# Kernel tuning notes

Measured on AMD Instinct MI355X. Metric: run time of the kernel, lower is better.

The kernel has to match this reference:

```python
import jax, jax.numpy as jnp
import numpy as np

N = 100_000   # num_nodes
D = 64        # emb_dim
E = 1_600_000 # num edges (before self loops)
L = 3         # n_layers
NEG_SLOPE = 0.2


def setup_inputs() -> dict:
    key = jax.random.key(0)
    ks = jax.random.split(key, 6)
    edge_index = jax.random.randint(ks[0], (2, E), 0, N, dtype=jnp.int32)
    # xavier-ish init for embedding and per-layer GATConv params
    emb = jax.random.normal(ks[1], (N, D), jnp.float32) * (1.0 / np.sqrt(D))
    W = jax.random.normal(ks[2], (L, D, D), jnp.float32) * (1.0 / np.sqrt(D))
    att_src = jax.random.normal(ks[3], (L, D), jnp.float32) * 0.1
    att_dst = jax.random.normal(ks[4], (L, D), jnp.float32) * 0.1
    bias = jnp.zeros((L, D), jnp.float32)
    return {"edge_index": edge_index, "emb": emb, "W": W,
            "att_src": att_src, "att_dst": att_dst, "bias": bias}


def _gat_layer(x, src, dst, W, a_s, a_d, b):
    # PyG GATConv, heads=1, concat=False, self-loops already in (src, dst)
    h = x @ W                                   # [N, D]
    e_s = h @ a_s                               # [N] per-node src score
    e_d = h @ a_d                               # [N] per-node dst score
    e = jax.nn.leaky_relu(e_s[src] + e_d[dst], NEG_SLOPE)   # [E']
    # segment softmax grouped by destination node (max is detached in PyG)
    m = jax.lax.stop_gradient(jax.ops.segment_max(e, dst, num_segments=N))
    ex = jnp.exp(e - m[dst])
    denom = jax.ops.segment_sum(ex, dst, num_segments=N)
    alpha = ex / (denom[dst] + 1e-16)           # [E']
    out = jax.ops.segment_sum(alpha[:, None] * h[src], dst, num_segments=N)
    return out + b


def reference(edge_index, emb, W, att_src, att_dst, bias):
    loops = jnp.arange(N, dtype=edge_index.dtype)
    src = jnp.concatenate([edge_index[0], loops])
    dst = jnp.concatenate([edge_index[1], loops])
    x = emb
    outs = [x]
    for l in range(L):
        x = jax.nn.elu(_gat_layer(x, src, dst, W[l], att_src[l], att_dst[l], bias[l]))
        outs.append(x)
    return jnp.mean(jnp.stack(outs, axis=0), axis=0)  # [N, D]
```

## Files before the change

kernel.cpp:

```cpp
#include <hip/hip_runtime.h>
#include <hip/hip_bf16.h>


#define BSHIFT 9
#define NPB 512
#define COL_CAP 10240

typedef _Float16 v8h __attribute__((ext_vector_type(8)));
typedef float v4f __attribute__((ext_vector_type(4)));
typedef unsigned short u16x8 __attribute__((ext_vector_type(8)));

__device__ inline float bf2f(unsigned short u) {
    return __uint_as_float(((unsigned int)u) << 16);
}
__device__ inline unsigned short f2bf(float v) {
    __hip_bfloat16 b = __float2bfloat16(v);
    return *reinterpret_cast<unsigned short*>(&b);
}
__device__ inline unsigned short f2h_u(float v) {
    return __builtin_bit_cast(unsigned short, (_Float16)v);
}
__device__ inline float h2f_u(unsigned short u) {
    return (float)__builtin_bit_cast(_Float16, u);
}

__global__ __launch_bounds__(256) void detect_bf16_k(const unsigned int* raw, int* flag, int* ghist) {
    __shared__ int sc;
    if (threadIdx.x == 0) sc = 0;
    ghist[threadIdx.x] = 0;
    __syncthreads();
    int c = 0;
    for (int i = threadIdx.x; i < 4096; i += 256) {
        unsigned int b = (raw[i] >> 8) & 0x7Fu;
        if (b >= 0x3Bu && b <= 0x3Fu) c++;
    }
    atomicAdd(&sc, c);
    __syncthreads();
    if (threadIdx.x == 0) *flag = (sc > 2048) ? 1 : 0;
}

__device__ inline float load_in(const void* p, int i, int isbf) {
    if (isbf) return bf2f(((const unsigned short*)p)[i]);
    return ((const float*)p)[i];
}

__global__ __launch_bounds__(256) void conv_emb_k(const void* emb, unsigned short* x, float* outacc,
                                                  int n, const int* flag) {
    int i = blockIdx.x * 256 + threadIdx.x;
    if (i >= n) return;
    float v = load_in(emb, i, *flag);
    x[i] = f2h_u(v);
    outacc[i] = v;
}

__global__ __launch_bounds__(256) void conv_params_k(const void* W, const void* as_, const void* ad_,
                                                     const void* b_, unsigned short* Wh, float* asf,
                                                     float* adf, float* bf, int nw, int na,
                                                     const int* flag) {
    int i = blockIdx.x * 256 + threadIdx.x;
    int isbf = *flag;
    if (i < nw) Wh[i] = f2h_u(load_in(W, i, isbf));
    if (i < na) {
        asf[i] = load_in(as_, i, isbf);
        adf[i] = load_in(ad_, i, isbf);
        bf[i]  = load_in(b_,  i, isbf);
    }
}


__global__ __launch_bounds__(256) void hist_k(const int* dst, int* ghist, int E) {
    __shared__ int h[256];
    h[threadIdx.x] = 0;
    __syncthreads();
    int cs = blockIdx.x * 4096;
    int ce = min(cs + 4096, E);
    for (int i = cs + threadIdx.x; i < ce; i += 256)
        atomicAdd(&h[dst[i] >> BSHIFT], 1);
    __syncthreads();
    if (h[threadIdx.x]) atomicAdd(&ghist[threadIdx.x], h[threadIdx.x]);
}

__global__ __launch_bounds__(256) void scan_nb_k(const int* ghist, int* pairs_base, int* col_base,
                                                 int* cursor, int* rowptr, int N, int E, int NB) {
    __shared__ int s1[256], s2[256];
    int t = threadIdx.x;
    int hv = (t < NB) ? ghist[t] : 0;
    int npb = (t < NB) ? min(N - (t << BSHIFT), NPB) : 0;
    s1[t] = hv; s2[t] = hv + npb;
    __syncthreads();
    for (int off = 1; off < 256; off <<= 1) {
        int t1 = (t >= off) ? s1[t - off] : 0;
        int t2 = (t >= off) ? s2[t - off] : 0;
        __syncthreads();
        s1[t] += t1; s2[t] += t2;
        __syncthreads();
    }
    if (t < NB) {
        pairs_base[t] = s1[t] - hv;
        cursor[t]     = s1[t] - hv;
        col_base[t]   = s2[t] - (hv + npb);
    }
    if (t == 0) rowptr[N] = E + N;
}

__global__ __launch_bounds__(256) void partition_k(const int* __restrict__ src,
                                                   const int* __restrict__ dst,
                                                   int* cursor, uint2* __restrict__ pairs,
                                                   int E, int NB) {
    __shared__ int cnt[256], base[256], rk[256];
    int t = threadIdx.x;
    cnt[t] = 0; rk[t] = 0;
    __syncthreads();
    int cs = blockIdx.x * 4096;
    int ce = min(cs + 4096, E);
    for (int i = cs + t; i < ce; i += 256)
        atomicAdd(&cnt[dst[i] >> BSHIFT], 1);
    __syncthreads();
    if (t < NB && cnt[t]) base[t] = atomicAdd(&cursor[t], cnt[t]);
    __syncthreads();
    for (int i = cs + t; i < ce; i += 256) {
        int d = dst[i];
        int b = d >> BSHIFT;
        int r = atomicAdd(&rk[b], 1);
        pairs[base[b] + r] = make_uint2((unsigned)src[i], (unsigned)d);
    }
}

__global__ __launch_bounds__(512) void build_k(const uint2* __restrict__ pairs,
                                               const int* __restrict__ ghist,
                                               const int* __restrict__ pairs_base,
                                               const int* __restrict__ col_base,
                                               int* __restrict__ rowptr, int* __restrict__ col,
                                               int N) {
    __shared__ int cnt[512], cnt2[512], sc[512], off[513];
    __shared__ int col_lds[COL_CAP];
    int b = blockIdx.x, t = threadIdx.x;
    int nloc = min(N - (b << BSHIFT), NPB);
    int ne = ghist[b], pb = pairs_base[b], cb = col_base[b];
    cnt[t] = 0; cnt2[t] = 0;
    __syncthreads();
    for (int i = t; i < ne; i += 512)
        atomicAdd(&cnt[pairs[pb + i].y & (NPB - 1)], 1);
    __syncthreads();
    int v = cnt[t] + (t < nloc ? 1 : 0);
    sc[t] = v;
    __syncthreads();
    for (int o = 1; o < 512; o <<= 1) {
        int tv = (t >= o) ? sc[t - o] : 0;
        __syncthreads();
        sc[t] += tv;
        __syncthreads();
    }
    off[t + 1] = sc[t];
    if (t == 0) off[0] = 0;
    __syncthreads();
    if (t < nloc) rowptr[(b << BSHIFT) + t] = cb + off[t];
    int total = off[nloc];
    bool fit = (total <= COL_CAP);
    for (int i = t; i < ne; i += 512) {
        uint2 p = pairs[pb + i];
        int loc = p.y & (NPB - 1);
        int pos = off[loc] + atomicAdd(&cnt2[loc], 1);
        if (fit) col_lds[pos] = (int)p.x;
        else     col[cb + pos] = (int)p.x;
    }
    if (t < nloc) {
        int pos = off[t + 1] - 1;
        int sv = (b << BSHIFT) + t;
        if (fit) col_lds[pos] = sv;
        else     col[cb + pos] = sv;
    }
    __syncthreads();
    if (fit)
        for (int i = t; i < total; i += 512) col[cb + i] = col_lds[i];
}


__global__ __launch_bounds__(256) void gemm_k(const unsigned short* __restrict__ x,
                                              const unsigned short* __restrict__ Wh,
                                              const float* __restrict__ asv,
                                              const float* __restrict__ adv,
                                              unsigned short* __restrict__ h,
                                              float* __restrict__ es, float* __restrict__ ed,
                                              int n, int nblk, int nwaves) {
    int lane = threadIdx.x & 63;
    int gwave = (blockIdx.x * 256 + threadIdx.x) >> 6;
    int c = lane & 15, quad = lane >> 4;

    v8h b[4][2];
    #pragma unroll
    for (int t = 0; t < 4; ++t)
        #pragma unroll
        for (int kf = 0; kf < 2; ++kf)
            #pragma unroll
            for (int j = 0; j < 8; ++j)
                b[t][kf][j] = __builtin_bit_cast(_Float16,
                    Wh[(kf * 32 + quad * 8 + j) * 64 + t * 16 + c]);

    float as4[4], ad4[4];
    #pragma unroll
    for (int t = 0; t < 4; ++t) { as4[t] = asv[t * 16 + c]; ad4[t] = adv[t * 16 + c]; }

    for (int nb = gwave; nb < nblk; nb += nwaves) {
        int base = nb * 16;
        int m = base + c; if (m >= n) m = n - 1;
        const v8h a0 = *(const v8h*)(x + (size_t)m * 64 + quad * 8);
        const v8h a1 = *(const v8h*)(x + (size_t)m * 64 + 32 + quad * 8);
        v4f z = {0.f, 0.f, 0.f, 0.f};
        v4f acc[4];
        #pragma unroll
        for (int t = 0; t < 4; ++t) {
            acc[t] = __builtin_amdgcn_mfma_f32_16x16x32_f16(a0, b[t][0], z, 0, 0, 0);
            acc[t] = __builtin_amdgcn_mfma_f32_16x16x32_f16(a1, b[t][1], acc[t], 0, 0, 0);
        }
        float ps[4], pd[4];
        #pragma unroll
        for (int r = 0; r < 4; ++r) {
            ps[r] = acc[0][r] * as4[0] + acc[1][r] * as4[1] + acc[2][r] * as4[2] + acc[3][r] * as4[3];
            pd[r] = acc[0][r] * ad4[0] + acc[1][r] * ad4[1] + acc[2][r] * ad4[2] + acc[3][r] * ad4[3];
        }
        #pragma unroll
        for (int off = 1; off < 16; off <<= 1)
            #pragma unroll
            for (int r = 0; r < 4; ++r) {
                ps[r] += __shfl_xor(ps[r], off);
                pd[r] += __shfl_xor(pd[r], off);
            }
        #pragma unroll
        for (int t = 0; t < 4; ++t)
            #pragma unroll
            for (int r = 0; r < 4; ++r) {
                int row = base + quad * 4 + r;
                if (row < n) h[(size_t)row * 64 + t * 16 + c] = f2h_u(acc[t][r]);
            }
        if (c == 0) {
            #pragma unroll
            for (int r = 0; r < 4; ++r) {
                int row = base + quad * 4 + r;
                if (row < n) { es[row] = ps[r]; ed[row] = pd[r]; }
            }
        }
    }
}

__device__ inline float elu_f(float v) { return v > 0.f ? v : (__expf(v) - 1.f); }

__global__ __launch_bounds__(256) void agg_k(const unsigned short* __restrict__ h,
                                             const float* __restrict__ es,
                                             const float* __restrict__ ed, const int* __restrict__ rowptr,
                                             const int* __restrict__ col, const float* __restrict__ bias,
                                             unsigned short* __restrict__ x, float* __restrict__ outacc,
                                             void* __restrict__ out, const int* __restrict__ flag,
                                             int write_out, int n) {
    int gw = (blockIdx.x * 256 + threadIdx.x) >> 6;
    int lane = threadIdx.x & 63;
    if (gw >= n) return;
    int start = rowptr[gw], end = rowptr[gw + 1];
    int deg = end - start;
    float edd = ed[gw];

    if (deg <= 64) {
        int c = 0;
        float e = -1e30f;
        if (lane < deg) {
            c = col[start + lane];
            float t = es[c] + edd;
            e = t > 0.f ? t : 0.2f * t;
        }
        float m = e;
        #pragma unroll
        for (int off = 32; off; off >>= 1) m = fmaxf(m, __shfl_xor(m, off));
        float ex = (lane < deg) ? __expf(e - m) : 0.f;
        float sum = ex;
        #pragma unroll
        for (int off = 32; off; off >>= 1) sum += __shfl_xor(sum, off);
        float a = ex / (sum + 1e-16f);

        int g = lane >> 3, j = lane & 7;
        float acc[8];
        #pragma unroll
        for (int i = 0; i < 8; ++i) acc[i] = 0.f;
        for (int t = 0; t < deg; t += 8) {
            int idx = t + g;
            int   s  = __shfl(c, idx);
            float al = __shfl(a, idx);
            if (idx < deg) {
                const u16x8 hv = *(const u16x8*)(h + (size_t)s * 64 + j * 8);
                #pragma unroll
                for (int i = 0; i < 8; ++i)
                    acc[i] = fmaf(al, h2f_u(hv[i]), acc[i]);
            }
        }
        #pragma unroll
        for (int off = 8; off < 64; off <<= 1)
            #pragma unroll
            for (int i = 0; i < 8; ++i)
                acc[i] += __shfl_xor(acc[i], off);

        if (g == 0) {
            size_t base = (size_t)gw * 64 + j * 8;
            float y[8], oa[8];
            #pragma unroll
            for (int i = 0; i < 8; ++i) {
                y[i] = elu_f(acc[i] + bias[j * 8 + i]);
                oa[i] = outacc[base + i] + y[i];
            }
            if (write_out) {
                if (*flag) {
                    u16x8 o;
                    #pragma unroll
                    for (int i = 0; i < 8; ++i) o[i] = f2bf(oa[i] * 0.25f);
                    *(u16x8*)((unsigned short*)out + base) = o;
                } else {
                    float4 o0 = make_float4(oa[0] * 0.25f, oa[1] * 0.25f, oa[2] * 0.25f, oa[3] * 0.25f);
                    float4 o1 = make_float4(oa[4] * 0.25f, oa[5] * 0.25f, oa[6] * 0.25f, oa[7] * 0.25f);
                    *(float4*)((float*)out + base) = o0;
                    *(float4*)((float*)out + base + 4) = o1;
                }
            } else {
                u16x8 xo;
                #pragma unroll
                for (int i = 0; i < 8; ++i) xo[i] = f2h_u(y[i]);
                *(u16x8*)(x + base) = xo;
                float4 o0 = make_float4(oa[0], oa[1], oa[2], oa[3]);
                float4 o1 = make_float4(oa[4], oa[5], oa[6], oa[7]);
                *(float4*)(outacc + base) = o0;
                *(float4*)(outacc + base + 4) = o1;
            }
        }
    } else {
        float m = -1e30f;
        for (int k = start + lane; k < end; k += 64) {
            float e = es[col[k]] + edd;
            e = e > 0.f ? e : 0.2f * e;
            m = fmaxf(m, e);
        }
        #pragma unroll
        for (int off = 32; off; off >>= 1) m = fmaxf(m, __shfl_xor(m, off));
        float sum = 0.f;
        for (int k = start + lane; k < end; k += 64) {
            float e = es[col[k]] + edd;
            e = e > 0.f ? e : 0.2f * e;
            sum += __expf(e - m);
        }
        #pragma unroll
        for (int off = 32; off; off >>= 1) sum += __shfl_xor(sum, off);
        float inv = 1.f / (sum + 1e-16f);
        float acc = 0.f;
        for (int k = start; k < end; ++k) {
            int s = col[k];
            float e = es[s] + edd;
            e = e > 0.f ? e : 0.2f * e;
            float al = __expf(e - m) * inv;
            acc = fmaf(al, h2f_u(h[(size_t)s * 64 + lane]), acc);
        }
        size_t base = (size_t)gw * 64 + lane;
        float y = elu_f(acc + bias[lane]);
        float oa = outacc[base] + y;
        if (write_out) {
            if (*flag) ((unsigned short*)out)[base] = f2bf(oa * 0.25f);
            else       ((float*)out)[base] = oa * 0.25f;
        } else {
            x[base] = f2h_u(y);
            outacc[base] = oa;
        }
    }
}


extern "C" void kernel_launch(void* const* d_in, const int* in_sizes, int n_in,
                              void* d_out, int out_size, void* d_ws, size_t ws_size,
                              hipStream_t stream) {
    const int*  edge = (const int*)d_in[0];
    const void* emb  = d_in[1];
    const void* W    = d_in[2];
    const void* as_  = d_in[3];
    const void* ad_  = d_in[4];
    const void* b_   = d_in[5];

    const int E = in_sizes[0] / 2;
    const int N = in_sizes[1] / 64;
    const int L = in_sizes[2] / 4096;
    const int NB = (N + NPB - 1) >> BSHIFT;
    const size_t N64 = (size_t)N * 64;

    char* p = (char*)d_ws;
    auto take = [&](size_t bytes) { char* r = p; p += (bytes + 255) & ~(size_t)255; return r; };
    unsigned short* x = (unsigned short*)take(N64 * 2);
    unsigned short* h = (unsigned short*)take(N64 * 2);
    float* outacc  = (float*)take(N64 * 4);
    float* es      = (float*)take((size_t)N * 4);
    float* ed      = (float*)take((size_t)N * 4);
    unsigned short* Wh = (unsigned short*)take((size_t)L * 4096 * 2);
    float* asf     = (float*)take((size_t)L * 64 * 4);
    float* adf     = (float*)take((size_t)L * 64 * 4);
    float* bf      = (float*)take((size_t)L * 64 * 4);
    uint2* pairs   = (uint2*)take((size_t)E * 8);
    int* rowptr    = (int*)take((size_t)(N + 1) * 4);
    int* col       = (int*)take((size_t)(E + N) * 4);
    int* ghist     = (int*)take(256 * 4);
    int* pairs_base= (int*)take(256 * 4);
    int* col_base  = (int*)take(256 * 4);
    int* cursor    = (int*)take(256 * 4);
    int* flag      = (int*)take(4);

    const int* srcp = edge;
    const int* dstp = edge + E;
    int nchunk = (E + 4095) / 4096;

    detect_bf16_k<<<1, 256, 0, stream>>>((const unsigned int*)emb, flag, ghist);
    conv_emb_k<<<(int)((N64 + 255) / 256), 256, 0, stream>>>(emb, x, outacc, (int)N64, flag);
    conv_params_k<<<(L * 4096 + 255) / 256, 256, 0, stream>>>(W, as_, ad_, b_, Wh, asf, adf, bf,
                                                              L * 4096, L * 64, flag);

    hist_k<<<nchunk, 256, 0, stream>>>(dstp, ghist, E);
    scan_nb_k<<<1, 256, 0, stream>>>(ghist, pairs_base, col_base, cursor, rowptr, N, E, NB);
    partition_k<<<nchunk, 256, 0, stream>>>(srcp, dstp, cursor, pairs, E, NB);
    build_k<<<NB, 512, 0, stream>>>(pairs, ghist, pairs_base, col_base, rowptr, col, N);

    const int nblk = (N + 15) / 16;
    const int ggrid = 400;
    for (int l = 0; l < L; ++l) {
        gemm_k<<<ggrid, 256, 0, stream>>>(x, Wh + (size_t)l * 4096, asf + l * 64, adf + l * 64,
                                          h, es, ed, N, nblk, ggrid * 4);
        agg_k<<<(N + 3) / 4, 256, 0, stream>>>(h, es, ed, rowptr, col, bf + l * 64, x, outacc,
                                               d_out, flag, (l == L - 1) ? 1 : 0, N);
    }
}
```

Baseline: 371.6 us.

## Fold attention vectors into GEMM, store per-layer fp16 outputs, finalize mean once

Precomputes W·att_src and W·att_dst on the device and packs them as an extra MFMA B-fragment, so the GEMM yields es/ed directly instead of needing per-row shuffle reductions. Weights are pre-laid-out in fragment order so each lane loads them with vector loads. The fp32 running-mean accumulator read-modify-write in every aggregation is replaced by per-layer fp16 outputs, which one finalize kernel averages; x2 reuses the pairs buffer. It also unrolls the edge gather by two and raises the GEMM grid. The trade-off is that the mean is now computed from fp16-rounded values, and there is one extra kernel launch.

```diff
diff --git a/kernel.cpp b/kernel.cpp
--- a/kernel.cpp
+++ b/kernel.cpp
@@ -5,6 +5,7 @@
 #define BSHIFT 9
 #define NPB 512
 #define COL_CAP 10240
+#define FRAG_STRIDE 5120
 
 typedef _Float16 v8h __attribute__((ext_vector_type(8)));
 typedef float v4f __attribute__((ext_vector_type(4)));
@@ -44,27 +45,43 @@
     return ((const float*)p)[i];
 }
 
-__global__ __launch_bounds__(256) void conv_emb_k(const void* emb, unsigned short* x, float* outacc,
+__global__ __launch_bounds__(256) void conv_emb_k(const void* emb, unsigned short* x0,
                                                   int n, const int* flag) {
     int i = blockIdx.x * 256 + threadIdx.x;
     if (i >= n) return;
-    float v = load_in(emb, i, *flag);
-    x[i] = f2h_u(v);
-    outacc[i] = v;
+    x0[i] = f2h_u(load_in(emb, i, *flag));
 }
 
 __global__ __launch_bounds__(256) void conv_params_k(const void* W, const void* as_, const void* ad_,
-                                                     const void* b_, unsigned short* Wh, float* asf,
-                                                     float* adf, float* bf, int nw, int na,
-                                                     const int* flag) {
+                                                     const void* b_, unsigned short* Whf, float* bf,
+                                                     int L_, const int* flag) {
     int i = blockIdx.x * 256 + threadIdx.x;
     int isbf = *flag;
-    if (i < nw) Wh[i] = f2h_u(load_in(W, i, isbf));
-    if (i < na) {
-        asf[i] = load_in(as_, i, isbf);
-        adf[i] = load_in(ad_, i, isbf);
-        bf[i]  = load_in(b_,  i, isbf);
-    }
+    if (i < L_ * 4096) {
+        int l = i >> 12, rem = i & 4095;
+        int k = rem >> 6, c64 = rem & 63;
+        int t = c64 >> 4, c = c64 & 15;
+        int kf = k >> 5, quad = (k >> 3) & 3, j = k & 7;
+        int f = t * 2 + kf, lane = quad * 16 + c;
+        Whf[l * FRAG_STRIDE + (f * 64 + lane) * 8 + j] = f2h_u(load_in(W, i, isbf));
+    }
+    if (i < L_ * 1024) {
+        int l = i >> 10, r = i & 1023;
+        int kf = r >> 9, rr = r & 511;
+        int lane = rr >> 3, j = rr & 7;
+        int c = lane & 15, quad = lane >> 4;
+        int k = kf * 32 + quad * 8 + j;
+        float val = 0.f;
+        if (c < 2) {
+            const void* av = c ? ad_ : as_;
+            float dot = 0.f;
+            for (int cc = 0; cc < 64; ++cc)
+                dot += load_in(W, l * 4096 + k * 64 + cc, isbf) * load_in(av, l * 64 + cc, isbf);
+            val = dot;
+        }
+        Whf[l * FRAG_STRIDE + ((8 + kf) * 64 + lane) * 8 + j] = f2h_u(val);
+    }
+    if (i < L_ * 64) bf[i] = load_in(b_, i, isbf);
 }
 
 
@@ -177,9 +194,7 @@
 
 
 __global__ __launch_bounds__(256) void gemm_k(const unsigned short* __restrict__ x,
-                                              const unsigned short* __restrict__ Wh,
-                                              const float* __restrict__ asv,
-                                              const float* __restrict__ adv,
+                                              const unsigned short* __restrict__ Whf,
                                               unsigned short* __restrict__ h,
                                               float* __restrict__ es, float* __restrict__ ed,
                                               int n, int nblk, int nwaves) {
@@ -187,57 +202,32 @@
     int gwave = (blockIdx.x * 256 + threadIdx.x) >> 6;
     int c = lane & 15, quad = lane >> 4;
 
-    v8h b[4][2];
+    v8h bfr[10];
     #pragma unroll
-    for (int t = 0; t < 4; ++t)
-        #pragma unroll
-        for (int kf = 0; kf < 2; ++kf)
-            #pragma unroll
-            for (int j = 0; j < 8; ++j)
-                b[t][kf][j] = __builtin_bit_cast(_Float16,
-                    Wh[(kf * 32 + quad * 8 + j) * 64 + t * 16 + c]);
-
-    float as4[4], ad4[4];
-    #pragma unroll
-    for (int t = 0; t < 4; ++t) { as4[t] = asv[t * 16 + c]; ad4[t] = adv[t * 16 + c]; }
-
+    for (int f = 0; f < 10; ++f)
+        bfr[f] = *(const v8h*)(Whf + (size_t)(f * 64 + lane) * 8);
+
+    v4f z = {0.f, 0.f, 0.f, 0.f};
     for (int nb = gwave; nb < nblk; nb += nwaves) {
         int base = nb * 16;
         int m = base + c; if (m >= n) m = n - 1;
         const v8h a0 = *(const v8h*)(x + (size_t)m * 64 + quad * 8);
         const v8h a1 = *(const v8h*)(x + (size_t)m * 64 + 32 + quad * 8);
-        v4f z = {0.f, 0.f, 0.f, 0.f};
-        v4f acc[4];
-        #pragma unroll
-        for (int t = 0; t < 4; ++t) {
-            acc[t] = __builtin_amdgcn_mfma_f32_16x16x32_f16(a0, b[t][0], z, 0, 0, 0);
-            acc[t] = __builtin_amdgcn_mfma_f32_16x16x32_f16(a1, b[t][1], acc[t], 0, 0, 0);
-        }
-        float ps[4], pd[4];
+        v4f acc[5];
+        #pragma unroll
+        for (int t = 0; t < 5; ++t) {
+            acc[t] = __builtin_amdgcn_mfma_f32_16x16x32_f16(a0, bfr[2 * t], z, 0, 0, 0);
+            acc[t] = __builtin_amdgcn_mfma_f32_16x16x32_f16(a1, bfr[2 * t + 1], acc[t], 0, 0, 0);
+        }
         #pragma unroll
         for (int r = 0; r < 4; ++r) {
-            ps[r] = acc[0][r] * as4[0] + acc[1][r] * as4[1] + acc[2][r] * as4[2] + acc[3][r] * as4[3];
-            pd[r] = acc[0][r] * ad4[0] + acc[1][r] * ad4[1] + acc[2][r] * ad4[2] + acc[3][r] * ad4[3];
-        }
-        #pragma unroll
-        for (int off = 1; off < 16; off <<= 1)
-            #pragma unroll
-            for (int r = 0; r < 4; ++r) {
-                ps[r] += __shfl_xor(ps[r], off);
-                pd[r] += __shfl_xor(pd[r], off);
-            }
-        #pragma unroll
-        for (int t = 0; t < 4; ++t)
-            #pragma unroll
-            for (int r = 0; r < 4; ++r) {
-                int row = base + quad * 4 + r;
-                if (row < n) h[(size_t)row * 64 + t * 16 + c] = f2h_u(acc[t][r]);
-            }
-        if (c == 0) {
-            #pragma unroll
-            for (int r = 0; r < 4; ++r) {
-                int row = base + quad * 4 + r;
-                if (row < n) { es[row] = ps[r]; ed[row] = pd[r]; }
+            int row = base + quad * 4 + r;
+            if (row < n) {
+                #pragma unroll
+                for (int t = 0; t < 4; ++t)
+                    h[(size_t)row * 64 + t * 16 + c] = f2h_u(acc[t][r]);
+                if (c == 0) es[row] = acc[4][r];
+                if (c == 1) ed[row] = acc[4][r];
             }
         }
     }
@@ -249,9 +239,7 @@
                                              const float* __restrict__ es,
                                              const float* __restrict__ ed, const int* __restrict__ rowptr,
                                              const int* __restrict__ col, const float* __restrict__ bias,
-                                             unsigned short* __restrict__ x, float* __restrict__ outacc,
-                                             void* __restrict__ out, const int* __restrict__ flag,
-                                             int write_out, int n) {
+                                             unsigned short* __restrict__ xo, int n) {
     int gw = (blockIdx.x * 256 + threadIdx.x) >> 6;
     int lane = threadIdx.x & 63;
     if (gw >= n) return;
@@ -280,15 +268,21 @@
         float acc[8];
         #pragma unroll
         for (int i = 0; i < 8; ++i) acc[i] = 0.f;
-        for (int t = 0; t < deg; t += 8) {
-            int idx = t + g;
-            int   s  = __shfl(c, idx);
-            float al = __shfl(a, idx);
-            if (idx < deg) {
-                const u16x8 hv = *(const u16x8*)(h + (size_t)s * 64 + j * 8);
+        for (int t = 0; t < deg; t += 16) {
+            int i0 = t + g, i1 = t + 8 + g;
+            int   s0  = __shfl(c, i0), s1 = __shfl(c, i1);
+            float al0 = __shfl(a, i0), al1 = __shfl(a, i1);
+            bool p0 = i0 < deg, p1 = i1 < deg;
+            u16x8 hv0, hv1;
+            if (p0) hv0 = *(const u16x8*)(h + (size_t)s0 * 64 + j * 8);
+            if (p1) hv1 = *(const u16x8*)(h + (size_t)s1 * 64 + j * 8);
+            if (p0) {
                 #pragma unroll
-                for (int i = 0; i < 8; ++i)
-                    acc[i] = fmaf(al, h2f_u(hv[i]), acc[i]);
+                for (int i = 0; i < 8; ++i) acc[i] = fmaf(al0, h2f_u(hv0[i]), acc[i]);
+            }
+            if (p1) {
+                #pragma unroll
+                for (int i = 0; i < 8; ++i) acc[i] = fmaf(al1, h2f_u(hv1[i]), acc[i]);
             }
         }
         #pragma unroll
@@ -298,35 +292,11 @@
                 acc[i] += __shfl_xor(acc[i], off);
 
         if (g == 0) {
-            size_t base = (size_t)gw * 64 + j * 8;
-            float y[8], oa[8];
+            u16x8 o;
             #pragma unroll
-            for (int i = 0; i < 8; ++i) {
-                y[i] = elu_f(acc[i] + bias[j * 8 + i]);
-                oa[i] = outacc[base + i] + y[i];
-            }
-            if (write_out) {
-                if (*flag) {
-                    u16x8 o;
-                    #pragma unroll
-                    for (int i = 0; i < 8; ++i) o[i] = f2bf(oa[i] * 0.25f);
-                    *(u16x8*)((unsigned short*)out + base) = o;
-                } else {
-                    float4 o0 = make_float4(oa[0] * 0.25f, oa[1] * 0.25f, oa[2] * 0.25f, oa[3] * 0.25f);
-                    float4 o1 = make_float4(oa[4] * 0.25f, oa[5] * 0.25f, oa[6] * 0.25f, oa[7] * 0.25f);
-                    *(float4*)((float*)out + base) = o0;
-                    *(float4*)((float*)out + base + 4) = o1;
-                }
-            } else {
-                u16x8 xo;
-                #pragma unroll
-                for (int i = 0; i < 8; ++i) xo[i] = f2h_u(y[i]);
-                *(u16x8*)(x + base) = xo;
-                float4 o0 = make_float4(oa[0], oa[1], oa[2], oa[3]);
-                float4 o1 = make_float4(oa[4], oa[5], oa[6], oa[7]);
-                *(float4*)(outacc + base) = o0;
-                *(float4*)(outacc + base + 4) = o1;
-            }
+            for (int i = 0; i < 8; ++i)
+                o[i] = f2h_u(elu_f(acc[i] + bias[j * 8 + i]));
+            *(u16x8*)(xo + (size_t)gw * 64 + j * 8) = o;
         }
     } else {
         float m = -1e30f;
@@ -354,16 +324,36 @@
             float al = __expf(e - m) * inv;
             acc = fmaf(al, h2f_u(h[(size_t)s * 64 + lane]), acc);
         }
-        size_t base = (size_t)gw * 64 + lane;
-        float y = elu_f(acc + bias[lane]);
-        float oa = outacc[base] + y;
-        if (write_out) {
-            if (*flag) ((unsigned short*)out)[base] = f2bf(oa * 0.25f);
-            else       ((float*)out)[base] = oa * 0.25f;
-        } else {
-            x[base] = f2h_u(y);
-            outacc[base] = oa;
-        }
+        xo[(size_t)gw * 64 + lane] = f2h_u(elu_f(acc + bias[lane]));
+    }
+}
+
+__global__ __launch_bounds__(256) void finalize_k(const unsigned short* __restrict__ x0,
+                                                  const unsigned short* __restrict__ x1,
+                                                  const unsigned short* __restrict__ x2,
+                                                  const unsigned short* __restrict__ x3,
+                                                  void* __restrict__ out, const int* flag, int n8) {
+    int i = blockIdx.x * 256 + threadIdx.x;
+    if (i >= n8) return;
+    size_t base = (size_t)i * 8;
+    u16x8 a = *(const u16x8*)(x0 + base);
+    u16x8 b = *(const u16x8*)(x1 + base);
+    u16x8 c = *(const u16x8*)(x2 + base);
+    u16x8 d = *(const u16x8*)(x3 + base);
+    float v[8];
+    #pragma unroll
+    for (int k = 0; k < 8; ++k)
+        v[k] = (h2f_u(a[k]) + h2f_u(b[k]) + h2f_u(c[k]) + h2f_u(d[k])) * 0.25f;
+    if (*flag) {
+        u16x8 o;
+        #pragma unroll
+        for (int k = 0; k < 8; ++k) o[k] = f2bf(v[k]);
+        *(u16x8*)((unsigned short*)out + base) = o;
+    } else {
+        float4 o0 = make_float4(v[0], v[1], v[2], v[3]);
+        float4 o1 = make_float4(v[4], v[5], v[6], v[7]);
+        *(float4*)((float*)out + base) = o0;
+        *(float4*)((float*)out + base + 4) = o1;
     }
 }
 
@@ -386,16 +376,16 @@
 
     char* p = (char*)d_ws;
     auto take = [&](size_t bytes) { char* r = p; p += (bytes + 255) & ~(size_t)255; return r; };
-    unsigned short* x = (unsigned short*)take(N64 * 2);
-    unsigned short* h = (unsigned short*)take(N64 * 2);
-    float* outacc  = (float*)take(N64 * 4);
+    unsigned short* x0 = (unsigned short*)take(N64 * 2);
+    unsigned short* x1 = (unsigned short*)take(N64 * 2);
+    unsigned short* x3 = (unsigned short*)take(N64 * 2);
+    unsigned short* h  = (unsigned short*)take(N64 * 2);
+    uint2* pairs   = (uint2*)take((size_t)E * 8 > N64 * 2 ? (size_t)E * 8 : N64 * 2);
+    unsigned short* x2 = (unsigned short*)pairs;
     float* es      = (float*)take((size_t)N * 4);
     float* ed      = (float*)take((size_t)N * 4);
-    unsigned short* Wh = (unsigned short*)take((size_t)L * 4096 * 2);
-    float* asf     = (float*)take((size_t)L * 64 * 4);
-    float* adf     = (float*)take((size_t)L * 64 * 4);
+    unsigned short* Whf = (unsigned short*)take((size_t)L * FRAG_STRIDE * 2);
     float* bf      = (float*)take((size_t)L * 64 * 4);
-    uint2* pairs   = (uint2*)take((size_t)E * 8);
     int* rowptr    = (int*)take((size_t)(N + 1) * 4);
     int* col       = (int*)take((size_t)(E + N) * 4);
     int* ghist     = (int*)take(256 * 4);
@@ -409,9 +399,8 @@
     int nchunk = (E + 4095) / 4096;
 
     detect_bf16_k<<<1, 256, 0, stream>>>((const unsigned int*)emb, flag, ghist);
-    conv_emb_k<<<(int)((N64 + 255) / 256), 256, 0, stream>>>(emb, x, outacc, (int)N64, flag);
-    conv_params_k<<<(L * 4096 + 255) / 256, 256, 0, stream>>>(W, as_, ad_, b_, Wh, asf, adf, bf,
-                                                              L * 4096, L * 64, flag);
+    conv_emb_k<<<(int)((N64 + 255) / 256), 256, 0, stream>>>(emb, x0, (int)N64, flag);
+    conv_params_k<<<(L * 4096 + 255) / 256, 256, 0, stream>>>(W, as_, ad_, b_, Whf, bf, L, flag);
 
     hist_k<<<nchunk, 256, 0, stream>>>(dstp, ghist, E);
     scan_nb_k<<<1, 256, 0, stream>>>(ghist, pairs_base, col_base, cursor, rowptr, N, E, NB);
@@ -419,11 +408,13 @@
     build_k<<<NB, 512, 0, stream>>>(pairs, ghist, pairs_base, col_base, rowptr, col, N);
 
     const int nblk = (N + 15) / 16;
-    const int ggrid = 400;
+    const int ggrid = 512;
+    unsigned short* xs[4] = {x0, x1, x2, x3};
     for (int l = 0; l < L; ++l) {
-        gemm_k<<<ggrid, 256, 0, stream>>>(x, Wh + (size_t)l * 4096, asf + l * 64, adf + l * 64,
+        gemm_k<<<ggrid, 256, 0, stream>>>(xs[l], Whf + (size_t)l * FRAG_STRIDE,
                                           h, es, ed, N, nblk, ggrid * 4);
-        agg_k<<<(N + 3) / 4, 256, 0, stream>>>(h, es, ed, rowptr, col, bf + l * 64, x, outacc,
-                                               d_out, flag, (l == L - 1) ? 1 : 0, N);
-    }
-}
+        agg_k<<<(N + 3) / 4, 256, 0, stream>>>(h, es, ed, rowptr, col, bf + l * 64, xs[l + 1], N);
+    }
+    finalize_k<<<(int)((N64 / 8 + 255) / 256), 256, 0, stream>>>(x0, x1, x2, x3, d_out, flag,
+                                                                 (int)(N64 / 8));
+}
```

New measurement: 375.2 us. About the same (+1.0%).
